# Kernel optimization log

Hardware: AMD Instinct MI355X
Metric: run time of the kernel (lower is better)

The kernel has to match this reference:

```python
import jax, jax.numpy as jnp
import numpy as np
import math

N, E, D, H, L = 50000, 800000, 256, 8, 8
DK = D // H
DFF = 4 * D


def _layernorm(h, g, b, eps=1e-5):
    m = jnp.mean(h, axis=-1, keepdims=True)
    v = jnp.mean((h - m) ** 2, axis=-1, keepdims=True)
    return (h - m) * jax.lax.rsqrt(v + eps) * g + b


def setup_inputs() -> dict:
    key = jax.random.key(0)
    ks = jax.random.split(key, 16)
    s = 1.0 / math.sqrt(D)
    x = jax.random.normal(ks[0], (N, D), dtype=jnp.float32)
    # every node gets >=1 in-edge so z > 0 everywhere (as in real connected graphs)
    edge_src = jax.random.randint(ks[1], (E,), 0, N, dtype=jnp.int32)
    edge_dst = jnp.concatenate([
        jnp.arange(N, dtype=jnp.int32),
        jax.random.randint(ks[2], (E - N,), 0, N, dtype=jnp.int32),
    ])
    return {
        "x": x,
        "edge_src": edge_src,
        "edge_dst": edge_dst,
        "Wq": jax.random.normal(ks[3], (L, D, D), dtype=jnp.float32) * s,
        "bq": jnp.zeros((L, D), dtype=jnp.float32),
        "Wk": jax.random.normal(ks[4], (L, D, D), dtype=jnp.float32) * s,
        "Wv": jax.random.normal(ks[5], (L, D, D), dtype=jnp.float32) * s,
        "Wo": jax.random.normal(ks[6], (L, D, D), dtype=jnp.float32) * s,
        "bo": jnp.zeros((L, D), dtype=jnp.float32),
        "ln1_g": jnp.ones((L, D), dtype=jnp.float32),
        "ln1_b": jnp.zeros((L, D), dtype=jnp.float32),
        "W1": jax.random.normal(ks[7], (L, D, DFF), dtype=jnp.float32) * s,
        "b1": jnp.zeros((L, DFF), dtype=jnp.float32),
        "W2": jax.random.normal(ks[8], (L, DFF, D), dtype=jnp.float32) * (1.0 / math.sqrt(DFF)),
        "b2": jnp.zeros((L, D), dtype=jnp.float32),
        "ln2_g": jnp.ones((L, D), dtype=jnp.float32),
        "ln2_b": jnp.zeros((L, D), dtype=jnp.float32),
    }


def _layer(x, src, dst, Wq, bq, Wk, Wv, Wo, bo, g1, b1n, W1, b1, W2, b2, g2, b2n):
    n = x.shape[0]
    q = (x @ Wq + bq).reshape(n, H, DK)
    k = (x @ Wk).reshape(n, H, DK)
    v = (x @ Wv).reshape(n, H, DK)
    # edge score: src_dot_dst('k','q') -> [E, H]
    score = jnp.einsum('ehd,ehd->eh', k[src], q[dst])
    # scaled_exp: exp(clamp(score / sqrt(d_k), -5, 5))
    score = jnp.exp(jnp.clip(score / math.sqrt(DK), -5.0, 5.0))
    # u_mul_e + sum aggregation -> wv [N, H, DK]; copy_edge + sum -> z [N, H]
    msg = v[src] * score[:, :, None]
    wv = jax.ops.segment_sum(msg, dst, num_segments=n)
    z = jax.ops.segment_sum(score, dst, num_segments=n)
    o = (wv / z[:, :, None]).reshape(n, D)
    h = _layernorm(x + o @ Wo + bo, g1, b1n)
    # FFN with residual + layernorm
    ff = jax.nn.relu(h @ W1 + b1) @ W2 + b2
    return _layernorm(h + ff, g2, b2n)


def reference(x, edge_src, edge_dst, Wq, bq, Wk, Wv, Wo, bo, ln1_g, ln1_b,
              W1, b1, W2, b2, ln2_g, ln2_b):
    for i in range(L):
        x = _layer(x, edge_src, edge_dst, Wq[i], bq[i], Wk[i], Wv[i], Wo[i],
                   bo[i], ln1_g[i], ln1_b[i], W1[i], b1[i], W2[i], b2[i],
                   ln2_g[i], ln2_b[i])
    return x
```

## Files before the change

kernel.cpp:

```cpp
#include <hip/hip_runtime.h>
#include <cstdint>
#include <cstddef>

#define D 256
#define H 8
#define DFF 1024

typedef short s16x8 __attribute__((ext_vector_type(8)));
typedef float f32x4 __attribute__((ext_vector_type(4)));

static inline int cdiv(int a, int b) { return (a + b - 1) / b; }

__device__ inline uint16_t f2bf(float x) {
    unsigned u = __float_as_uint(x);
    u += 0x7FFFu + ((u >> 16) & 1u);
    return (uint16_t)(u >> 16);
}
__device__ inline float bf2f(uint16_t h) {
    return __uint_as_float(((unsigned)h) << 16);
}

__device__ inline void gload_lds16(const void* g, void* l) {
    __builtin_amdgcn_global_load_lds(
        (const __attribute__((address_space(1))) void*)g,
        (__attribute__((address_space(3))) void*)l, 16, 0, 0);
}

__global__ __launch_bounds__(256) void zero_int_kernel(int* __restrict__ p, int count)
{
    int i = blockIdx.x * blockDim.x + threadIdx.x;
    if (i < count) p[i] = 0;
}

__global__ __launch_bounds__(256) void count_deg_kernel(
    const int* __restrict__ edst, int* __restrict__ deg, int E)
{
    int e = blockIdx.x * blockDim.x + threadIdx.x;
    if (e < E) atomicAdd(&deg[edst[e]], 1);
}

__global__ __launch_bounds__(256) void block_sum_kernel(
    const int* __restrict__ deg, int* __restrict__ bsum, int N)
{
    int t = threadIdx.x;
    int gid = blockIdx.x * 256 + t;
    int val = (gid < N) ? deg[gid] : 0;
    #pragma unroll
    for (int o = 1; o < 64; o <<= 1) val += __shfl_xor(val, o);
    __shared__ int r[4];
    if ((t & 63) == 0) r[t >> 6] = val;
    __syncthreads();
    if (t == 0) bsum[blockIdx.x] = r[0] + r[1] + r[2] + r[3];
}

__global__ __launch_bounds__(256) void scan_bsum_kernel(int* __restrict__ bsum, int nb)
{
    __shared__ int tmp[256];
    int t = threadIdx.x;
    int val = (t < nb) ? bsum[t] : 0;
    tmp[t] = val;
    __syncthreads();
    for (int off = 1; off < 256; off <<= 1) {
        int add = (t >= off) ? tmp[t - off] : 0;
        __syncthreads();
        tmp[t] += add;
        __syncthreads();
    }
    if (t < nb) bsum[t] = tmp[t] - val;
}

__global__ __launch_bounds__(256) void scan_write_kernel(
    const int* __restrict__ deg, const int* __restrict__ bsum,
    int* __restrict__ rowptr, int* __restrict__ cursor, int N)
{
    __shared__ int tmp[256];
    int t = threadIdx.x;
    int gid = blockIdx.x * 256 + t;
    int val = (gid < N) ? deg[gid] : 0;
    tmp[t] = val;
    __syncthreads();
    for (int off = 1; off < 256; off <<= 1) {
        int add = (t >= off) ? tmp[t - off] : 0;
        __syncthreads();
        tmp[t] += add;
        __syncthreads();
    }
    int excl = tmp[t] - val + bsum[blockIdx.x];
    if (gid < N) { rowptr[gid] = excl; cursor[gid] = excl; }
    if (gid == N - 1) rowptr[N] = excl + val;
}

__global__ __launch_bounds__(256) void fill_csr_kernel(
    const int* __restrict__ esrc, const int* __restrict__ edst,
    int* __restrict__ cursor, int* __restrict__ csr_src, int E)
{
    int e = blockIdx.x * blockDim.x + threadIdx.x;
    if (e < E) {
        int pos = atomicAdd(&cursor[edst[e]], 1);
        csr_src[pos] = esrc[e];
    }
}

__global__ __launch_bounds__(256) void transpose_cast_kernel(
    const float* __restrict__ in, uint16_t* __restrict__ out,
    int R, int C, size_t inLS, size_t outLS)
{
    __shared__ float t[32][33];
    in  += blockIdx.z * inLS;
    out += blockIdx.z * outLS;
    int c0 = blockIdx.x * 32, r0 = blockIdx.y * 32;
    int tx = threadIdx.x, ty = threadIdx.y;
    #pragma unroll
    for (int i = 0; i < 4; ++i)
        t[ty + i * 8][tx] = in[(size_t)(r0 + ty + i * 8) * C + c0 + tx];
    __syncthreads();
    #pragma unroll
    for (int i = 0; i < 4; ++i)
        out[(size_t)(c0 + ty + i * 8) * R + r0 + tx] = f2bf(t[tx][ty + i * 8]);
}

__global__ __launch_bounds__(256) void cast_f32_bf16_kernel(
    const float* __restrict__ in, uint16_t* __restrict__ out, int n4)
{
    int i = blockIdx.x * blockDim.x + threadIdx.x;
    if (i >= n4) return;
    float4 f = ((const float4*)in)[i];
    uint16_t o0 = f2bf(f.x), o1 = f2bf(f.y), o2 = f2bf(f.z), o3 = f2bf(f.w);
    uint2 pk;
    pk.x = (unsigned)o0 | ((unsigned)o1 << 16);
    pk.y = (unsigned)o2 | ((unsigned)o3 << 16);
    ((uint2*)out)[i] = pk;
}

__global__ __launch_bounds__(256) void build_qkv_bias_kernel(
    const float* __restrict__ bq, float* __restrict__ qb, int total)
{
    int i = blockIdx.x * blockDim.x + threadIdx.x;
    if (i >= total) return;
    int l = i / 768, c = i - l * 768;
    qb[i] = (c < 256) ? bq[l * 256 + c] : 0.f;
}

__global__ __launch_bounds__(256) void gemm_bf16_kernel(
    const uint16_t* __restrict__ A, int lda, int M, int K,
    const uint16_t* __restrict__ BT, int Nc,
    const float* __restrict__ bias,
    uint16_t* __restrict__ Cb, int relu)
{
    __shared__ __align__(16) uint16_t As[128 * 32];
    __shared__ __align__(16) uint16_t Bs[128 * 32];

    const int tid  = threadIdx.x;
    const int lane = tid & 63;
    const int w    = tid >> 6;
    const int wr   = w >> 1, wc = w & 1;
    const int quad = lane >> 4;
    const int l15  = lane & 15;

    const int m0 = blockIdx.x * 128;
    const int n0 = blockIdx.y * 128;

    f32x4 acc[4][4] = {};

    const int jbase = w * 2;
    const int srow  = lane >> 2;
    const int skc   = (lane & 3) * 8;

    for (int k0 = 0; k0 < K; k0 += 32) {
        #pragma unroll
        for (int jj = 0; jj < 2; ++jj) {
            int j = jbase + jj;
            int r = j * 16 + srow;
            int gr = m0 + r; if (gr > M - 1) gr = M - 1;
            gload_lds16(A  + (size_t)gr * lda + k0 + skc, &As[j * 512]);
            gload_lds16(BT + (size_t)(n0 + r) * K + k0 + skc, &Bs[j * 512]);
        }
        __syncthreads();

        s16x8 af[4], bf[4];
        #pragma unroll
        for (int t = 0; t < 4; ++t) {
            af[t] = *(const s16x8*)&As[(wr * 64 + t * 16 + l15) * 32 + quad * 8];
            bf[t] = *(const s16x8*)&Bs[(wc * 64 + t * 16 + l15) * 32 + quad * 8];
        }
        #pragma unroll
        for (int i = 0; i < 4; ++i)
            #pragma unroll
            for (int jt = 0; jt < 4; ++jt)
                acc[i][jt] = __builtin_amdgcn_mfma_f32_16x16x32_bf16(
                    af[i], bf[jt], acc[i][jt], 0, 0, 0);
        __syncthreads();
    }

    float bv[4];
    #pragma unroll
    for (int jt = 0; jt < 4; ++jt)
        bv[jt] = bias ? bias[n0 + wc * 64 + jt * 16 + l15] : 0.f;

    #pragma unroll
    for (int i = 0; i < 4; ++i) {
        #pragma unroll
        for (int r = 0; r < 4; ++r) {
            int m = m0 + wr * 64 + i * 16 + quad * 4 + r;
            if (m >= M) continue;
            #pragma unroll
            for (int jt = 0; jt < 4; ++jt) {
                int n = n0 + wc * 64 + jt * 16 + l15;
                float val = acc[i][jt][r] + bv[jt];
                if (relu) val = fmaxf(val, 0.f);
                Cb[(size_t)m * Nc + n] = f2bf(val);
            }
        }
    }
}

__global__ __launch_bounds__(256) void gemm_ln_kernel(
    const uint16_t* __restrict__ A, int lda, int M, int K,
    const uint16_t* __restrict__ BT,
    const float* __restrict__ bias,
    const float* __restrict__ resid,
    const float* __restrict__ g, const float* __restrict__ b,
    float* __restrict__ Cf, uint16_t* __restrict__ Cb)
{
    __shared__ __align__(16) uint16_t As[64 * 32];
    __shared__ __align__(16) uint16_t Bs[256 * 32];
    __shared__ float sS[64][4];
    __shared__ float sQ[64][4];

    const int tid  = threadIdx.x;
    const int lane = tid & 63;
    const int w    = tid >> 6;
    const int quad = lane >> 4;
    const int l15  = lane & 15;

    const int m0 = blockIdx.x * 64;

    f32x4 acc[4][4] = {};

    for (int k0 = 0; k0 < K; k0 += 32) {
        {
            int slot = tid;
            int r = slot >> 2, kc = (slot & 3) * 8;
            int gr = m0 + r; if (gr > M - 1) gr = M - 1;
            gload_lds16(A + (size_t)gr * lda + k0 + kc, &As[slot * 8]);
        }
        #pragma unroll
        for (int i = 0; i < 4; ++i) {
            int slot = i * 256 + tid;
            int n = slot >> 2, kc = (slot & 3) * 8;
            gload_lds16(BT + (size_t)n * K + k0 + kc, &Bs[slot * 8]);
        }
        __syncthreads();

        s16x8 af[4], bf[4];
        #pragma unroll
        for (int t = 0; t < 4; ++t) {
            af[t] = *(const s16x8*)&As[(t * 16 + l15) * 32 + quad * 8];
            bf[t] = *(const s16x8*)&Bs[(w * 64 + t * 16 + l15) * 32 + quad * 8];
        }
        #pragma unroll
        for (int i = 0; i < 4; ++i)
            #pragma unroll
            for (int jt = 0; jt < 4; ++jt)
                acc[i][jt] = __builtin_amdgcn_mfma_f32_16x16x32_bf16(
                    af[i], bf[jt], acc[i][jt], 0, 0, 0);
        __syncthreads();
    }

    float bv[4], gv[4], bbv[4];
    #pragma unroll
    for (int jt = 0; jt < 4; ++jt) {
        int n = w * 64 + jt * 16 + l15;
        bv[jt]  = bias[n];
        gv[jt]  = g[n];
        bbv[jt] = b[n];
    }

    #pragma unroll
    for (int i = 0; i < 4; ++i) {
        #pragma unroll
        for (int r = 0; r < 4; ++r) {
            int ml = i * 16 + quad * 4 + r;
            int m  = m0 + ml;
            bool valid = (m < M);
            float s = 0.f, s2 = 0.f;
            #pragma unroll
            for (int jt = 0; jt < 4; ++jt) {
                int n = w * 64 + jt * 16 + l15;
                float val = acc[i][jt][r] + bv[jt];
                if (valid) val += resid[(size_t)m * 256 + n];
                acc[i][jt][r] = val;
                s += val;
                s2 += val * val;
            }
            #pragma unroll
            for (int o = 1; o < 16; o <<= 1) {
                s  += __shfl_xor(s, o);
                s2 += __shfl_xor(s2, o);
            }
            if (l15 == 0) { sS[ml][w] = s; sQ[ml][w] = s2; }
        }
    }
    __syncthreads();

    #pragma unroll
    for (int i = 0; i < 4; ++i) {
        #pragma unroll
        for (int r = 0; r < 4; ++r) {
            int ml = i * 16 + quad * 4 + r;
            int m  = m0 + ml;
            if (m >= M) continue;
            float s  = sS[ml][0] + sS[ml][1] + sS[ml][2] + sS[ml][3];
            float s2 = sQ[ml][0] + sQ[ml][1] + sQ[ml][2] + sQ[ml][3];
            float mean = s * (1.f / 256.f);
            float var  = s2 * (1.f / 256.f) - mean * mean;
            float rstd = rsqrtf(var + 1e-5f);
            #pragma unroll
            for (int jt = 0; jt < 4; ++jt) {
                int n = w * 64 + jt * 16 + l15;
                float out = (acc[i][jt][r] - mean) * rstd * gv[jt] + bbv[jt];
                Cf[(size_t)m * 256 + n] = out;
                if (Cb) Cb[(size_t)m * 256 + n] = f2bf(out);
            }
        }
    }
}

__global__ __launch_bounds__(256) void node_attn_kernel(
    uint16_t* __restrict__ qkv,
    const int* __restrict__ rowptr, const int* __restrict__ csr_src, int N)
{
    int node = (blockIdx.x * blockDim.x + threadIdx.x) >> 6;
    int lane = threadIdx.x & 63;
    if (node >= N) return;

    uint16_t* qp = qkv + (size_t)node * 768 + lane * 4;
    uint2 qu = *(const uint2*)qp;
    float q0 = bf2f((uint16_t)(qu.x & 0xFFFF)), q1 = bf2f((uint16_t)(qu.x >> 16));
    float q2 = bf2f((uint16_t)(qu.y & 0xFFFF)), q3 = bf2f((uint16_t)(qu.y >> 16));

    float a0 = 0.f, a1 = 0.f, a2 = 0.f, a3 = 0.f, zacc = 0.f;
    const float inv_sqrt_dk = 0.17677669529663687f;

    int beg = rowptr[node], end = rowptr[node + 1];
    int i = beg;
    for (; i + 1 < end; i += 2) {
        int s0 = csr_src[i], s1 = csr_src[i + 1];
        const uint16_t* b0 = qkv + (size_t)s0 * 768;
        const uint16_t* b1 = qkv + (size_t)s1 * 768;
        uint2 ku0 = *(const uint2*)(b0 + 256 + lane * 4);
        uint2 ku1 = *(const uint2*)(b1 + 256 + lane * 4);
        uint2 vu0 = *(const uint2*)(b0 + 512 + lane * 4);
        uint2 vu1 = *(const uint2*)(b1 + 512 + lane * 4);

        float p0 = bf2f((uint16_t)(ku0.x & 0xFFFF)) * q0
                 + bf2f((uint16_t)(ku0.x >> 16))   * q1
                 + bf2f((uint16_t)(ku0.y & 0xFFFF)) * q2
                 + bf2f((uint16_t)(ku0.y >> 16))   * q3;
        float p1 = bf2f((uint16_t)(ku1.x & 0xFFFF)) * q0
                 + bf2f((uint16_t)(ku1.x >> 16))   * q1
                 + bf2f((uint16_t)(ku1.y & 0xFFFF)) * q2
                 + bf2f((uint16_t)(ku1.y >> 16))   * q3;
        p0 += __shfl_xor(p0, 1); p1 += __shfl_xor(p1, 1);
        p0 += __shfl_xor(p0, 2); p1 += __shfl_xor(p1, 2);
        p0 += __shfl_xor(p0, 4); p1 += __shfl_xor(p1, 4);
        float sc0 = __expf(fminf(fmaxf(p0 * inv_sqrt_dk, -5.f), 5.f));
        float sc1 = __expf(fminf(fmaxf(p1 * inv_sqrt_dk, -5.f), 5.f));

        a0 += bf2f((uint16_t)(vu0.x & 0xFFFF)) * sc0;
        a1 += bf2f((uint16_t)(vu0.x >> 16))   * sc0;
        a2 += bf2f((uint16_t)(vu0.y & 0xFFFF)) * sc0;
        a3 += bf2f((uint16_t)(vu0.y >> 16))   * sc0;
        zacc += sc0;
        a0 += bf2f((uint16_t)(vu1.x & 0xFFFF)) * sc1;
        a1 += bf2f((uint16_t)(vu1.x >> 16))   * sc1;
        a2 += bf2f((uint16_t)(vu1.y & 0xFFFF)) * sc1;
        a3 += bf2f((uint16_t)(vu1.y >> 16))   * sc1;
        zacc += sc1;
    }
    if (i < end) {
        int s = csr_src[i];
        const uint16_t* base = qkv + (size_t)s * 768;
        uint2 ku = *(const uint2*)(base + 256 + lane * 4);
        float p = bf2f((uint16_t)(ku.x & 0xFFFF)) * q0
                + bf2f((uint16_t)(ku.x >> 16))   * q1
                + bf2f((uint16_t)(ku.y & 0xFFFF)) * q2
                + bf2f((uint16_t)(ku.y >> 16))   * q3;
        p += __shfl_xor(p, 1);
        p += __shfl_xor(p, 2);
        p += __shfl_xor(p, 4);
        float sc = __expf(fminf(fmaxf(p * inv_sqrt_dk, -5.f), 5.f));
        uint2 vu = *(const uint2*)(base + 512 + lane * 4);
        a0 += bf2f((uint16_t)(vu.x & 0xFFFF)) * sc;
        a1 += bf2f((uint16_t)(vu.x >> 16))   * sc;
        a2 += bf2f((uint16_t)(vu.y & 0xFFFF)) * sc;
        a3 += bf2f((uint16_t)(vu.y >> 16))   * sc;
        zacc += sc;
    }
    float inv = 1.f / zacc;
    uint2 pk;
    pk.x = (unsigned)f2bf(a0 * inv) | ((unsigned)f2bf(a1 * inv) << 16);
    pk.y = (unsigned)f2bf(a2 * inv) | ((unsigned)f2bf(a3 * inv) << 16);
    *(uint2*)qp = pk;
}

extern "C" void kernel_launch(void* const* d_in, const int* in_sizes, int n_in,
                              void* d_out, int out_size, void* d_ws, size_t ws_size,
                              hipStream_t stream)
{
    const float* x0   = (const float*)d_in[0];
    const int* esrc   = (const int*)d_in[1];
    const int* edst   = (const int*)d_in[2];
    const float* Wq   = (const float*)d_in[3];
    const float* bq   = (const float*)d_in[4];
    const float* Wk   = (const float*)d_in[5];
    const float* Wv   = (const float*)d_in[6];
    const float* Wo   = (const float*)d_in[7];
    const float* bo   = (const float*)d_in[8];
    const float* ln1g = (const float*)d_in[9];
    const float* ln1b = (const float*)d_in[10];
    const float* W1   = (const float*)d_in[11];
    const float* b1   = (const float*)d_in[12];
    const float* W2   = (const float*)d_in[13];
    const float* b2   = (const float*)d_in[14];
    const float* ln2g = (const float*)d_in[15];
    const float* ln2b = (const float*)d_in[16];

    const int N = in_sizes[0] / D;
    const int E = in_sizes[1];
    const int L = in_sizes[3] / (D * D);
    const size_t ND = (size_t)N * D;

    char* p = (char*)d_ws;
    float* bufX = (float*)p;         p += ND * 4;
    uint16_t* xb  = (uint16_t*)p;
    uint16_t* t1  = xb;              p += ND * 2;
    uint16_t* qkv = (uint16_t*)p;    p += (size_t)N * 768 * 2;
    uint16_t* hb  = (uint16_t*)p;    p += ND * 2;
    uint16_t* BTqkv = (uint16_t*)p;  p += (size_t)L * 768 * 256 * 2;
    uint16_t* BTo   = (uint16_t*)p;  p += (size_t)L * 256 * 256 * 2;
    uint16_t* BT1   = (uint16_t*)p;  p += (size_t)L * 1024 * 256 * 2;
    uint16_t* BT2   = (uint16_t*)p;  p += (size_t)L * 256 * 1024 * 2;
    float* qbias    = (float*)p;     p += (size_t)L * 768 * 4;
    int* rowptr  = (int*)p;          p += (size_t)(N + 1) * 4;
    int* cursor  = (int*)p;          p += (size_t)N * 4;
    int* deg     = cursor;
    int* csr_src = (int*)p;          p += (size_t)E * 4;
    int* bsum    = (int*)p;

    const int nb = cdiv(N, 256);
    dim3 blk(256);
    int edgeBlocks = cdiv(E, 256);
    int nodeBlocks = cdiv(N, 4);

    dim3 tb(32, 8);
    transpose_cast_kernel<<<dim3(8, 8, L), tb, 0, stream>>>(Wq, BTqkv, 256, 256, (size_t)65536, (size_t)768 * 256);
    transpose_cast_kernel<<<dim3(8, 8, L), tb, 0, stream>>>(Wk, BTqkv + 256 * 256, 256, 256, (size_t)65536, (size_t)768 * 256);
    transpose_cast_kernel<<<dim3(8, 8, L), tb, 0, stream>>>(Wv, BTqkv + 512 * 256, 256, 256, (size_t)65536, (size_t)768 * 256);
    transpose_cast_kernel<<<dim3(8, 8, L), tb, 0, stream>>>(Wo, BTo, 256, 256, (size_t)65536, (size_t)65536);
    transpose_cast_kernel<<<dim3(32, 8, L), tb, 0, stream>>>(W1, BT1, 256, 1024, (size_t)262144, (size_t)262144);
    transpose_cast_kernel<<<dim3(8, 32, L), tb, 0, stream>>>(W2, BT2, 1024, 256, (size_t)262144, (size_t)262144);
    build_qkv_bias_kernel<<<cdiv(L * 768, 256), blk, 0, stream>>>(bq, qbias, L * 768);
    cast_f32_bf16_kernel<<<cdiv((int)(ND / 4), 256), blk, 0, stream>>>(x0, xb, (int)(ND / 4));

    zero_int_kernel<<<cdiv(N, 256), blk, 0, stream>>>(deg, N);
    count_deg_kernel<<<edgeBlocks, blk, 0, stream>>>(edst, deg, E);
    block_sum_kernel<<<nb, blk, 0, stream>>>(deg, bsum, N);
    scan_bsum_kernel<<<1, blk, 0, stream>>>(bsum, nb);
    scan_write_kernel<<<nb, blk, 0, stream>>>(deg, bsum, rowptr, cursor, N);
    fill_csr_kernel<<<edgeBlocks, blk, 0, stream>>>(esrc, edst, cursor, csr_src, E);

    const int Mt128 = cdiv(N, 128);
    const int Mt64  = cdiv(N, 64);
    dim3 gQKV(Mt128, 768 / 128);
    dim3 gF1(Mt128, 1024 / 128);
    dim3 gLN(Mt64, 1);

    for (int l = 0; l < L; ++l) {
        const uint16_t* BTqkv_l = BTqkv + (size_t)l * 768 * 256;
        const uint16_t* BTo_l   = BTo + (size_t)l * 65536;
        const uint16_t* BT1_l   = BT1 + (size_t)l * 262144;
        const uint16_t* BT2_l   = BT2 + (size_t)l * 262144;
        const float* xin_f = (l == 0) ? x0 : bufX;

        gemm_bf16_kernel<<<gQKV, blk, 0, stream>>>(xb, 256, N, 256, BTqkv_l, 768,
            qbias + (size_t)l * 768, qkv, 0);

        node_attn_kernel<<<nodeBlocks, blk, 0, stream>>>(qkv, rowptr, csr_src, N);

        gemm_ln_kernel<<<gLN, blk, 0, stream>>>(qkv, 768, N, 256, BTo_l,
            bo + (size_t)l * 256, xin_f, ln1g + (size_t)l * 256, ln1b + (size_t)l * 256,
            bufX, hb);

        gemm_bf16_kernel<<<gF1, blk, 0, stream>>>(hb, 256, N, 256, BT1_l, 1024,
            b1 + (size_t)l * 1024, t1, 1);

        float* fout = (l == L - 1) ? (float*)d_out : bufX;
        gemm_ln_kernel<<<gLN, blk, 0, stream>>>(t1, 1024, N, 1024, BT2_l,
            b2 + (size_t)l * 256, bufX, ln2g + (size_t)l * 256, ln2b + (size_t)l * 256,
            fout, (l == L - 1) ? nullptr : xb);

        xin_f = bufX;
    }
}
```

Baseline: 3.423 ms.

## Split QKV into separate buffers, store V as FP8, widen GEMM tiles

The QKV projection now writes Q and K as separate bf16 arrays and V as an fp8 array. This shrinks the rows gathered per edge in the attention kernel and packs them more tightly. The generic GEMM moves to a 128x256 tile with launch bounds of 2 blocks per SM, which reuses each A tile across more columns and halves the grid in the column direction. FP8 storage of V lowers precision and may affect accuracy. The larger accumulator array raises register pressure.

```diff
diff --git a/kernel.cpp b/kernel.cpp
--- a/kernel.cpp
+++ b/kernel.cpp
@@ -8,6 +8,7 @@
 
 typedef short s16x8 __attribute__((ext_vector_type(8)));
 typedef float f32x4 __attribute__((ext_vector_type(4)));
+typedef float f32x2 __attribute__((ext_vector_type(2)));
 
 static inline int cdiv(int a, int b) { return (a + b - 1) / b; }
 
@@ -18,6 +19,10 @@
 }
 __device__ inline float bf2f(uint16_t h) {
     return __uint_as_float(((unsigned)h) << 16);
+}
+__device__ inline uint8_t f2fp8(float x) {
+    int pk = __builtin_amdgcn_cvt_pk_fp8_f32(x, x, 0, false);
+    return (uint8_t)(pk & 0xFF);
 }
 
 __device__ inline void gload_lds16(const void* g, void* l) {
@@ -141,50 +146,52 @@
     qb[i] = (c < 256) ? bq[l * 256 + c] : 0.f;
 }
 
-__global__ __launch_bounds__(256) void gemm_bf16_kernel(
+__global__ __launch_bounds__(256, 2) void gemm128_kernel(
     const uint16_t* __restrict__ A, int lda, int M, int K,
-    const uint16_t* __restrict__ BT, int Nc,
+    const uint16_t* __restrict__ BT,
     const float* __restrict__ bias,
-    uint16_t* __restrict__ Cb, int relu)
+    int qkv_mode,
+    uint16_t* __restrict__ q, uint16_t* __restrict__ kb, uint8_t* __restrict__ v8,
+    uint16_t* __restrict__ Cstd, int Nstd, int relu)
 {
     __shared__ __align__(16) uint16_t As[128 * 32];
-    __shared__ __align__(16) uint16_t Bs[128 * 32];
+    __shared__ __align__(16) uint16_t Bs[256 * 32];
 
     const int tid  = threadIdx.x;
     const int lane = tid & 63;
     const int w    = tid >> 6;
-    const int wr   = w >> 1, wc = w & 1;
     const int quad = lane >> 4;
     const int l15  = lane & 15;
-
-    const int m0 = blockIdx.x * 128;
-    const int n0 = blockIdx.y * 128;
-
-    f32x4 acc[4][4] = {};
-
-    const int jbase = w * 2;
-    const int srow  = lane >> 2;
-    const int skc   = (lane & 3) * 8;
+    const int m0   = blockIdx.x * 128;
+    const int col0 = blockIdx.y * 256;
+
+    f32x4 acc[8][4] = {};
+
+    const int r_a = tid >> 2;
+    const int kc  = (tid & 3) * 8;
 
     for (int k0 = 0; k0 < K; k0 += 32) {
         #pragma unroll
-        for (int jj = 0; jj < 2; ++jj) {
-            int j = jbase + jj;
-            int r = j * 16 + srow;
-            int gr = m0 + r; if (gr > M - 1) gr = M - 1;
-            gload_lds16(A  + (size_t)gr * lda + k0 + skc, &As[j * 512]);
-            gload_lds16(BT + (size_t)(n0 + r) * K + k0 + skc, &Bs[j * 512]);
-        }
-        __syncthreads();
-
-        s16x8 af[4], bf[4];
-        #pragma unroll
-        for (int t = 0; t < 4; ++t) {
-            af[t] = *(const s16x8*)&As[(wr * 64 + t * 16 + l15) * 32 + quad * 8];
-            bf[t] = *(const s16x8*)&Bs[(wc * 64 + t * 16 + l15) * 32 + quad * 8];
-        }
-        #pragma unroll
-        for (int i = 0; i < 4; ++i)
+        for (int j = 0; j < 2; ++j) {
+            int gr = m0 + j * 64 + r_a; if (gr > M - 1) gr = M - 1;
+            gload_lds16(A + (size_t)gr * lda + k0 + kc, &As[(j * 256 + tid) * 8]);
+        }
+        #pragma unroll
+        for (int j = 0; j < 4; ++j) {
+            int n = j * 64 + r_a;
+            gload_lds16(BT + (size_t)(col0 + n) * K + k0 + kc, &Bs[(j * 256 + tid) * 8]);
+        }
+        __syncthreads();
+
+        s16x8 af[8], bf[4];
+        #pragma unroll
+        for (int i = 0; i < 8; ++i)
+            af[i] = *(const s16x8*)&As[(i * 16 + l15) * 32 + quad * 8];
+        #pragma unroll
+        for (int jt = 0; jt < 4; ++jt)
+            bf[jt] = *(const s16x8*)&Bs[(w * 64 + jt * 16 + l15) * 32 + quad * 8];
+        #pragma unroll
+        for (int i = 0; i < 8; ++i)
             #pragma unroll
             for (int jt = 0; jt < 4; ++jt)
                 acc[i][jt] = __builtin_amdgcn_mfma_f32_16x16x32_bf16(
@@ -195,20 +202,26 @@
     float bv[4];
     #pragma unroll
     for (int jt = 0; jt < 4; ++jt)
-        bv[jt] = bias ? bias[n0 + wc * 64 + jt * 16 + l15] : 0.f;
-
-    #pragma unroll
-    for (int i = 0; i < 4; ++i) {
+        bv[jt] = bias[col0 + w * 64 + jt * 16 + l15];
+
+    #pragma unroll
+    for (int i = 0; i < 8; ++i) {
         #pragma unroll
         for (int r = 0; r < 4; ++r) {
-            int m = m0 + wr * 64 + i * 16 + quad * 4 + r;
+            int m = m0 + i * 16 + quad * 4 + r;
             if (m >= M) continue;
             #pragma unroll
             for (int jt = 0; jt < 4; ++jt) {
-                int n = n0 + wc * 64 + jt * 16 + l15;
+                int nl = w * 64 + jt * 16 + l15;
                 float val = acc[i][jt][r] + bv[jt];
                 if (relu) val = fmaxf(val, 0.f);
-                Cb[(size_t)m * Nc + n] = f2bf(val);
+                if (qkv_mode) {
+                    if (blockIdx.y == 0)      q [(size_t)m * 256 + nl] = f2bf(val);
+                    else if (blockIdx.y == 1) kb[(size_t)m * 256 + nl] = f2bf(val);
+                    else                      v8[(size_t)m * 256 + nl] = f2fp8(val);
+                } else {
+                    Cstd[(size_t)m * Nstd + col0 + nl] = f2bf(val);
+                }
             }
         }
     }
@@ -327,14 +340,15 @@
 }
 
 __global__ __launch_bounds__(256) void node_attn_kernel(
-    uint16_t* __restrict__ qkv,
+    uint16_t* __restrict__ q, const uint16_t* __restrict__ kb,
+    const uint8_t* __restrict__ v8,
     const int* __restrict__ rowptr, const int* __restrict__ csr_src, int N)
 {
     int node = (blockIdx.x * blockDim.x + threadIdx.x) >> 6;
     int lane = threadIdx.x & 63;
     if (node >= N) return;
 
-    uint16_t* qp = qkv + (size_t)node * 768 + lane * 4;
+    uint16_t* qp = q + (size_t)node * 256 + lane * 4;
     uint2 qu = *(const uint2*)qp;
     float q0 = bf2f((uint16_t)(qu.x & 0xFFFF)), q1 = bf2f((uint16_t)(qu.x >> 16));
     float q2 = bf2f((uint16_t)(qu.y & 0xFFFF)), q3 = bf2f((uint16_t)(qu.y >> 16));
@@ -346,12 +360,10 @@
     int i = beg;
     for (; i + 1 < end; i += 2) {
         int s0 = csr_src[i], s1 = csr_src[i + 1];
-        const uint16_t* b0 = qkv + (size_t)s0 * 768;
-        const uint16_t* b1 = qkv + (size_t)s1 * 768;
-        uint2 ku0 = *(const uint2*)(b0 + 256 + lane * 4);
-        uint2 ku1 = *(const uint2*)(b1 + 256 + lane * 4);
-        uint2 vu0 = *(const uint2*)(b0 + 512 + lane * 4);
-        uint2 vu1 = *(const uint2*)(b1 + 512 + lane * 4);
+        uint2 ku0 = *(const uint2*)(kb + (size_t)s0 * 256 + lane * 4);
+        uint2 ku1 = *(const uint2*)(kb + (size_t)s1 * 256 + lane * 4);
+        unsigned vu0 = *(const unsigned*)(v8 + (size_t)s0 * 256 + lane * 4);
+        unsigned vu1 = *(const unsigned*)(v8 + (size_t)s1 * 256 + lane * 4);
 
         float p0 = bf2f((uint16_t)(ku0.x & 0xFFFF)) * q0
                  + bf2f((uint16_t)(ku0.x >> 16))   * q1
@@ -367,21 +379,21 @@
         float sc0 = __expf(fminf(fmaxf(p0 * inv_sqrt_dk, -5.f), 5.f));
         float sc1 = __expf(fminf(fmaxf(p1 * inv_sqrt_dk, -5.f), 5.f));
 
-        a0 += bf2f((uint16_t)(vu0.x & 0xFFFF)) * sc0;
-        a1 += bf2f((uint16_t)(vu0.x >> 16))   * sc0;
-        a2 += bf2f((uint16_t)(vu0.y & 0xFFFF)) * sc0;
-        a3 += bf2f((uint16_t)(vu0.y >> 16))   * sc0;
-        zacc += sc0;
-        a0 += bf2f((uint16_t)(vu1.x & 0xFFFF)) * sc1;
-        a1 += bf2f((uint16_t)(vu1.x >> 16))   * sc1;
-        a2 += bf2f((uint16_t)(vu1.y & 0xFFFF)) * sc1;
-        a3 += bf2f((uint16_t)(vu1.y >> 16))   * sc1;
-        zacc += sc1;
+        f32x2 vA0 = __builtin_amdgcn_cvt_pk_f32_fp8(vu0, false);
+        f32x2 vB0 = __builtin_amdgcn_cvt_pk_f32_fp8(vu0, true);
+        f32x2 vA1 = __builtin_amdgcn_cvt_pk_f32_fp8(vu1, false);
+        f32x2 vB1 = __builtin_amdgcn_cvt_pk_f32_fp8(vu1, true);
+
+        a0 += vA0[0] * sc0 + vA1[0] * sc1;
+        a1 += vA0[1] * sc0 + vA1[1] * sc1;
+        a2 += vB0[0] * sc0 + vB1[0] * sc1;
+        a3 += vB0[1] * sc0 + vB1[1] * sc1;
+        zacc += sc0 + sc1;
     }
     if (i < end) {
         int s = csr_src[i];
-        const uint16_t* base = qkv + (size_t)s * 768;
-        uint2 ku = *(const uint2*)(base + 256 + lane * 4);
+        uint2 ku = *(const uint2*)(kb + (size_t)s * 256 + lane * 4);
+        unsigned vu = *(const unsigned*)(v8 + (size_t)s * 256 + lane * 4);
         float p = bf2f((uint16_t)(ku.x & 0xFFFF)) * q0
                 + bf2f((uint16_t)(ku.x >> 16))   * q1
                 + bf2f((uint16_t)(ku.y & 0xFFFF)) * q2
@@ -390,11 +402,12 @@
         p += __shfl_xor(p, 2);
         p += __shfl_xor(p, 4);
         float sc = __expf(fminf(fmaxf(p * inv_sqrt_dk, -5.f), 5.f));
-        uint2 vu = *(const uint2*)(base + 512 + lane * 4);
-        a0 += bf2f((uint16_t)(vu.x & 0xFFFF)) * sc;
-        a1 += bf2f((uint16_t)(vu.x >> 16))   * sc;
-        a2 += bf2f((uint16_t)(vu.y & 0xFFFF)) * sc;
-        a3 += bf2f((uint16_t)(vu.y >> 16))   * sc;
+        f32x2 vA = __builtin_amdgcn_cvt_pk_f32_fp8(vu, false);
+        f32x2 vB = __builtin_amdgcn_cvt_pk_f32_fp8(vu, true);
+        a0 += vA[0] * sc;
+        a1 += vA[1] * sc;
+        a2 += vB[0] * sc;
+        a3 += vB[1] * sc;
         zacc += sc;
     }
     float inv = 1.f / zacc;
@@ -432,20 +445,23 @@
     const size_t ND = (size_t)N * D;
 
     char* p = (char*)d_ws;
-    float* bufX = (float*)p;         p += ND * 4;
-    uint16_t* xb  = (uint16_t*)p;
-    uint16_t* t1  = xb;              p += ND * 2;
-    uint16_t* qkv = (uint16_t*)p;    p += (size_t)N * 768 * 2;
-    uint16_t* hb  = (uint16_t*)p;    p += ND * 2;
-    uint16_t* BTqkv = (uint16_t*)p;  p += (size_t)L * 768 * 256 * 2;
-    uint16_t* BTo   = (uint16_t*)p;  p += (size_t)L * 256 * 256 * 2;
-    uint16_t* BT1   = (uint16_t*)p;  p += (size_t)L * 1024 * 256 * 2;
-    uint16_t* BT2   = (uint16_t*)p;  p += (size_t)L * 256 * 1024 * 2;
-    float* qbias    = (float*)p;     p += (size_t)L * 768 * 4;
-    int* rowptr  = (int*)p;          p += (size_t)(N + 1) * 4;
-    int* cursor  = (int*)p;          p += (size_t)N * 4;
+    float* bufX   = (float*)p;     p += ND * 4;
+    uint16_t* xb  = (uint16_t*)p;  p += ND * 2;
+    uint16_t* q   = (uint16_t*)p;  p += ND * 2;
+    uint16_t* kb  = (uint16_t*)p;  p += ND * 2;
+    uint8_t*  v8  = (uint8_t*)p;   p += ND;
+    p += ND * 3;
+    uint16_t* t1  = q;
+    uint16_t* hb  = (uint16_t*)p;  p += ND * 2;
+    uint16_t* BTqkv = (uint16_t*)p; p += (size_t)L * 768 * 256 * 2;
+    uint16_t* BTo   = (uint16_t*)p; p += (size_t)L * 256 * 256 * 2;
+    uint16_t* BT1   = (uint16_t*)p; p += (size_t)L * 1024 * 256 * 2;
+    uint16_t* BT2   = (uint16_t*)p; p += (size_t)L * 256 * 1024 * 2;
+    float* qbias    = (float*)p;    p += (size_t)L * 768 * 4;
+    int* rowptr  = (int*)p;         p += (size_t)(N + 1) * 4;
+    int* cursor  = (int*)p;         p += (size_t)N * 4;
     int* deg     = cursor;
-    int* csr_src = (int*)p;          p += (size_t)E * 4;
+    int* csr_src = (int*)p;         p += (size_t)E * 4;
     int* bsum    = (int*)p;
 
     const int nb = cdiv(N, 256);
@@ -472,8 +488,8 @@
 
     const int Mt128 = cdiv(N, 128);
     const int Mt64  = cdiv(N, 64);
-    dim3 gQKV(Mt128, 768 / 128);
-    dim3 gF1(Mt128, 1024 / 128);
+    dim3 gQKV(Mt128, 3);
+    dim3 gF1(Mt128, 4);
     dim3 gLN(Mt64, 1);
 
     for (int l = 0; l < L; ++l) {
@@ -483,23 +499,21 @@
         const uint16_t* BT2_l   = BT2 + (size_t)l * 262144;
         const float* xin_f = (l == 0) ? x0 : bufX;
 
-        gemm_bf16_kernel<<<gQKV, blk, 0, stream>>>(xb, 256, N, 256, BTqkv_l, 768,
-            qbias + (size_t)l * 768, qkv, 0);
-
-        node_attn_kernel<<<nodeBlocks, blk, 0, stream>>>(qkv, rowptr, csr_src, N);
-
-        gemm_ln_kernel<<<gLN, blk, 0, stream>>>(qkv, 768, N, 256, BTo_l,
+        gemm128_kernel<<<gQKV, blk, 0, stream>>>(xb, 256, N, 256, BTqkv_l,
+            qbias + (size_t)l * 768, 1, q, kb, v8, nullptr, 0, 0);
+
+        node_attn_kernel<<<nodeBlocks, blk, 0, stream>>>(q, kb, v8, rowptr, csr_src, N);
+
+        gemm_ln_kernel<<<gLN, blk, 0, stream>>>(q, 256, N, 256, BTo_l,
             bo + (size_t)l * 256, xin_f, ln1g + (size_t)l * 256, ln1b + (size_t)l * 256,
             bufX, hb);
 
-        gemm_bf16_kernel<<<gF1, blk, 0, stream>>>(hb, 256, N, 256, BT1_l, 1024,
-            b1 + (size_t)l * 1024, t1, 1);
+        gemm128_kernel<<<gF1, blk, 0, stream>>>(hb, 256, N, 256, BT1_l,
+            b1 + (size_t)l * 1024, 0, nullptr, nullptr, nullptr, t1, 1024, 1);
 
         float* fout = (l == L - 1) ? (float*)d_out : bufX;
         gemm_ln_kernel<<<gLN, blk, 0, stream>>>(t1, 1024, N, 1024, BT2_l,
             b2 + (size_t)l * 256, bufX, ln2g + (size_t)l * 256, ln2b + (size_t)l * 256,
             fout, (l == L - 1) ? nullptr : xb);
-
-        xin_f = bufX;
-    }
-}
+    }
+}
```

New measurement: 3.687 ms. 1.08x slower.
